# Performance work log

Measured on AMD Instinct MI355X. Metric: run time of the kernel, lower is better.

The kernel has to match this reference:

```python
import jax, jax.numpy as jnp
import numpy as np

DROPOUT_P = 0.5


def setup_inputs() -> dict:
    key = jax.random.key(0)
    ks = jax.random.split(key, 8)
    N, F0 = 10000, 1024
    s = lambda k, shp, fan: jax.random.normal(k, shp, jnp.float32) / np.sqrt(fan)
    return {
        "x": jax.random.normal(ks[0], (N, F0), jnp.float32),
        "adj": jax.random.uniform(ks[1], (N, N), jnp.float32),
        "W1": s(ks[2], (F0, 512), F0),
        "b1": jnp.zeros((512,), jnp.float32),
        "W2": s(ks[3], (512, 256), 512),
        "b2": jnp.zeros((256,), jnp.float32),
        "W3": s(ks[4], (256, 128), 256),
        "b3": jnp.zeros((128,), jnp.float32),
    }


def _gc(x, adj, W, b):
    # GraphConvolution: adj @ (x @ W) + b
    return adj @ (x @ W) + b


def reference(x, adj, W1, b1, W2, b2, W3, b3):
    x1 = jax.nn.relu(_gc(x, adj, W1, b1))
    # F.dropout(x1, p) with training=True: mask + 1/(1-p) scaling; fixed key for determinism
    keep = jax.random.bernoulli(jax.random.key(42), 1.0 - DROPOUT_P, x1.shape)
    x1 = jnp.where(keep, x1 / (1.0 - DROPOUT_P), 0.0)
    x2 = _gc(x1, adj, W2, b2)
    x3 = _gc(x2, adj, W3, b3)
    return x3
```

## Files before the change

kernel.cpp:

```cpp
#include <hip/hip_runtime.h>
#include <hip/hip_bf16.h>
#include <stdint.h>


#define MROWS 10000
#define KPAD  10016

typedef __attribute__((ext_vector_type(8))) short short8;
typedef __attribute__((ext_vector_type(4))) float floatx4;

__device__ __forceinline__ unsigned short f2bf(float f) {
  union { float f; unsigned u; } v; v.f = f;
  unsigned u = v.u;
  u += 0x7fffu + ((u >> 16) & 1u);
  return (unsigned short)(u >> 16);
}

__device__ __forceinline__ bool dropout_keep(unsigned i) {
  const unsigned halfn = 2560000u;
  const unsigned j = (i < halfn) ? i : (i - halfn);
  unsigned x0 = j, x1 = j + halfn;
  const unsigned k0 = 0u, k1 = 42u, k2 = 0u ^ 42u ^ 0x1BD11BDAu;
  x0 += k0; x1 += k1;
#define TFR(r) { x0 += x1; x1 = (x1 << (r)) | (x1 >> (32 - (r))); x1 ^= x0; }
  TFR(13) TFR(15) TFR(26) TFR(6)   x0 += k1; x1 += k2 + 1u;
  TFR(17) TFR(29) TFR(16) TFR(24)  x0 += k2; x1 += k0 + 2u;
  TFR(13) TFR(15) TFR(26) TFR(6)   x0 += k0; x1 += k1 + 3u;
  TFR(17) TFR(29) TFR(16) TFR(24)  x0 += k1; x1 += k2 + 4u;
  TFR(13) TFR(15) TFR(26) TFR(6)   x0 += k2; x1 += k0 + 5u;
#undef TFR
  const unsigned bits = (i < halfn) ? x0 : x1;
  return bits < 0x80000000u;
}

__global__ void cast_adj_kernel(const float* __restrict__ in, unsigned short* __restrict__ out) {
  const int q = blockIdx.x * blockDim.x + threadIdx.x;
  const int row = blockIdx.y;
  if (q >= 2504) return;
  const int col = q * 4;
  ushort4 o;
  if (col < 10000) {
    const float4 v = *(const float4*)(in + (size_t)row * 10000 + col);
    o.x = f2bf(v.x); o.y = f2bf(v.y); o.z = f2bf(v.z); o.w = f2bf(v.w);
  } else {
    o.x = 0; o.y = 0; o.z = 0; o.w = 0;
  }
  *(ushort4*)(out + (size_t)row * KPAD + col) = o;
}

__global__ void cast_vec_kernel(const float* __restrict__ in, unsigned short* __restrict__ out, int n4) {
  const int id = blockIdx.x * blockDim.x + threadIdx.x;
  if (id >= n4) return;
  const float4 v = ((const float4*)in)[id];
  ushort4 o; o.x = f2bf(v.x); o.y = f2bf(v.y); o.z = f2bf(v.z); o.w = f2bf(v.w);
  ((ushort4*)out)[id] = o;
}

__global__ void castT_kernel(const float* __restrict__ in, unsigned short* __restrict__ out, int K, int N) {
  const int id = blockIdx.x * blockDim.x + threadIdx.x;
  if (id >= K * N) return;
  const int n = id / K, k = id % K;
  out[(size_t)n * K + k] = f2bf(in[(size_t)k * N + n]);
}

__global__ void zero_pad_kernel(unsigned short* __restrict__ p, int rows) {
  const int id = blockIdx.x * blockDim.x + threadIdx.x;
  if (id >= rows * 16) return;
  const int r = id >> 4, c = id & 15;
  p[(size_t)r * KPAD + 10000 + c] = 0;
}

template<int OUT_KIND, int EPI>
__global__ __launch_bounds__(256, 2) void gemm_mfma(
    const unsigned short* __restrict__ A, int lda,
    const unsigned short* __restrict__ BT, int ldb,
    void* __restrict__ Cv, int ldc,
    const float* __restrict__ bias,
    int M, int N, int K,
    int chunk)
{
  __shared__ unsigned short As[128 * 32];
  __shared__ unsigned short Bs[128 * 32];

  const int tid  = threadIdx.x;
  const int lane = tid & 63;
  const int wave = tid >> 6;
  const int m0 = blockIdx.y * 128;
  const int n0 = blockIdx.x * 128;
  const int wm = (wave & 1) * 64;
  const int wn = (wave >> 1) * 64;

  int kstart = 0, kend = K;
  if (OUT_KIND == 3) {
    kstart = blockIdx.z * chunk;
    kend   = kstart + chunk; if (kend > K) kend = K;
  }

  floatx4 acc[4][4];
#pragma unroll
  for (int i = 0; i < 4; ++i)
#pragma unroll
    for (int j = 0; j < 4; ++j) acc[i][j] = (floatx4){0.f, 0.f, 0.f, 0.f};

  const int c1 = tid, c2 = tid + 256;
  int ar1 = m0 + (c1 >> 2); if (ar1 > M - 1) ar1 = M - 1;
  int ar2 = m0 + (c2 >> 2); if (ar2 > M - 1) ar2 = M - 1;
  const int br1 = n0 + (c1 >> 2);
  const int br2 = n0 + (c2 >> 2);
  const unsigned short* aG1 = A  + (size_t)ar1 * lda + (c1 & 3) * 8;
  const unsigned short* aG2 = A  + (size_t)ar2 * lda + (c2 & 3) * 8;
  const unsigned short* bG1 = BT + (size_t)br1 * ldb + (c1 & 3) * 8;
  const unsigned short* bG2 = BT + (size_t)br2 * ldb + (c2 & 3) * 8;
  unsigned short* lA1 = As + c1 * 8;
  unsigned short* lA2 = As + c2 * 8;
  unsigned short* lB1 = Bs + c1 * 8;
  unsigned short* lB2 = Bs + c2 * 8;

  const int fr = lane & 15;
  const int fq = (lane >> 4) * 8;

#define GLL16(g, l) __builtin_amdgcn_global_load_lds( \
    (const __attribute__((address_space(1))) void*)(g), \
    (__attribute__((address_space(3))) void*)(l), 16, 0, 0)

  for (int k0 = kstart; k0 < kend; k0 += 32) {
    GLL16(aG1 + k0, lA1);
    GLL16(aG2 + k0, lA2);
    GLL16(bG1 + k0, lB1);
    GLL16(bG2 + k0, lB2);
    __syncthreads();
    short8 af[4], bfv[4];
#pragma unroll
    for (int mi = 0; mi < 4; ++mi)
      af[mi] = *(const short8*)(As + (wm + mi * 16 + fr) * 32 + fq);
#pragma unroll
    for (int ni = 0; ni < 4; ++ni)
      bfv[ni] = *(const short8*)(Bs + (wn + ni * 16 + fr) * 32 + fq);
#pragma unroll
    for (int mi = 0; mi < 4; ++mi)
#pragma unroll
      for (int ni = 0; ni < 4; ++ni)
        acc[mi][ni] = __builtin_amdgcn_mfma_f32_16x16x32_bf16(af[mi], bfv[ni], acc[mi][ni], 0, 0, 0);
    __syncthreads();
  }
#undef GLL16

  if (OUT_KIND == 0) {
    unsigned short* Ct = (unsigned short*)Cv;
#pragma unroll
    for (int mi = 0; mi < 4; ++mi) {
      const int mbase = m0 + wm + mi * 16 + (lane >> 4) * 4;
      if (mbase < M) {
#pragma unroll
        for (int ni = 0; ni < 4; ++ni) {
          const int n = n0 + wn + ni * 16 + fr;
          ushort4 o;
          o.x = f2bf(acc[mi][ni][0]);
          o.y = f2bf(acc[mi][ni][1]);
          o.z = f2bf(acc[mi][ni][2]);
          o.w = f2bf(acc[mi][ni][3]);
          *(ushort4*)(Ct + (size_t)n * ldc + mbase) = o;
        }
      }
    }
  } else if (OUT_KIND == 3) {
    float* P = (float*)Cv + (size_t)blockIdx.z * (size_t)M * (size_t)N;
#pragma unroll
    for (int ni = 0; ni < 4; ++ni) {
      const int col = n0 + wn + ni * 16 + fr;
#pragma unroll
      for (int mi = 0; mi < 4; ++mi) {
        const int rbase = m0 + wm + mi * 16 + (lane >> 4) * 4;
#pragma unroll
        for (int r = 0; r < 4; ++r) {
          const int row = rbase + r;
          if (row < M) P[(size_t)row * N + col] = acc[mi][ni][r];
        }
      }
    }
  } else {
#pragma unroll
    for (int ni = 0; ni < 4; ++ni) {
      const int col = n0 + wn + ni * 16 + fr;
      const float bv = (EPI >= 1) ? bias[col] : 0.0f;
#pragma unroll
      for (int mi = 0; mi < 4; ++mi) {
        const int rbase = m0 + wm + mi * 16 + (lane >> 4) * 4;
#pragma unroll
        for (int r = 0; r < 4; ++r) {
          const int row = rbase + r;
          if (row < M) {
            float v = acc[mi][ni][r] + bv;
            if (EPI == 2) {
              v = v > 0.f ? v : 0.f;
              const unsigned idx = (unsigned)row * (unsigned)N + (unsigned)col;
              v = dropout_keep(idx) ? v * 2.0f : 0.0f;
            }
            if (OUT_KIND == 2)
              ((float*)Cv)[(size_t)row * ldc + col] = v;
            else
              ((unsigned short*)Cv)[(size_t)row * ldc + col] = f2bf(v);
          }
        }
      }
    }
  }
}

template<int EPI>
__global__ void reduce_epi_kernel(const float* __restrict__ P, void* __restrict__ outv,
                                  const float* __restrict__ bias,
                                  int S, int total4, unsigned nmask, size_t MN) {
  const int t = blockIdx.x * blockDim.x + threadIdx.x;
  if (t >= total4) return;
  const size_t off = (size_t)t * 4;
  float4 a = *(const float4*)(P + off);
  for (int s = 1; s < S; ++s) {
    const float4 b = *(const float4*)(P + (size_t)s * MN + off);
    a.x += b.x; a.y += b.y; a.z += b.z; a.w += b.w;
  }
  const unsigned col = (unsigned)off & nmask;
  a.x += bias[col]; a.y += bias[col + 1]; a.z += bias[col + 2]; a.w += bias[col + 3];
  if (EPI == 2) {
    float* e = &a.x;
#pragma unroll
    for (int j = 0; j < 4; ++j) {
      float v = e[j] > 0.f ? e[j] : 0.f;
      e[j] = dropout_keep((unsigned)off + j) ? v * 2.0f : 0.0f;
    }
  }
  if (EPI == 3) {
    *(float4*)((float*)outv + off) = a;
  } else {
    ushort4 o;
    o.x = f2bf(a.x); o.y = f2bf(a.y); o.z = f2bf(a.z); o.w = f2bf(a.w);
    *(ushort4*)((unsigned short*)outv + off) = o;
  }
}

static inline int pick_split(size_t avail, size_t per_split, int target) {
  int s = 1;
  while (s < target && (size_t)(s * 2) * per_split <= avail) s *= 2;
  return s;
}

extern "C" void kernel_launch(void* const* d_in, const int* in_sizes, int n_in,
                              void* d_out, int out_size, void* d_ws, size_t ws_size,
                              hipStream_t stream) {
  const float* x   = (const float*)d_in[0];
  const float* adj = (const float*)d_in[1];
  const float* W1  = (const float*)d_in[2];
  const float* b1  = (const float*)d_in[3];
  const float* W2  = (const float*)d_in[4];
  const float* b2  = (const float*)d_in[5];
  const float* W3  = (const float*)d_in[6];
  const float* b3  = (const float*)d_in[7];
  float* out = (float*)d_out;

  char* ws = (char*)d_ws;
  unsigned short* adjb = (unsigned short*)(ws);
  unsigned short* xb   = (unsigned short*)(ws + 200320000ull);
  unsigned short* w1t  = (unsigned short*)(ws + 220800000ull);
  unsigned short* w2t  = (unsigned short*)(ws + 221848576ull);
  unsigned short* w3t  = (unsigned short*)(ws + 222110720ull);
  unsigned short* h1t  = (unsigned short*)(ws + 222176256ull);
  unsigned short* x1   = (unsigned short*)(ws + 232432640ull);
  unsigned short* h2t  = (unsigned short*)(ws + 242672640ull);
  unsigned short* x2   = (unsigned short*)(ws + 247800832ull);
  unsigned short* h3t  = (unsigned short*)(ws + 252920832ull);
  float*          P    = (float*)(ws + 255484928ull);
  const size_t avail = (ws_size > 255484928ull) ? ws_size - 255484928ull : 0;

  const int S1 = pick_split(avail, 20480000ull, 4);
  const int S2 = pick_split(avail, 10240000ull, 8);
  const int S3 = pick_split(avail,  5120000ull, 16);

  cast_adj_kernel<<<dim3(10, 10000), 256, 0, stream>>>(adj, adjb);
  cast_vec_kernel<<<10000, 256, 0, stream>>>(x, xb, 2560000);
  castT_kernel<<<2048, 256, 0, stream>>>(W1, w1t, 1024, 512);
  castT_kernel<<<512, 256, 0, stream>>>(W2, w2t, 512, 256);
  castT_kernel<<<128, 256, 0, stream>>>(W3, w3t, 256, 128);
  zero_pad_kernel<<<32, 256, 0, stream>>>(h1t, 512);
  zero_pad_kernel<<<16, 256, 0, stream>>>(h2t, 256);
  zero_pad_kernel<<<8, 256, 0, stream>>>(h3t, 128);

  gemm_mfma<0, 0><<<dim3(4, 79), 256, 0, stream>>>(xb, 1024, w1t, 1024, h1t, KPAD, nullptr, MROWS, 512, 1024, 1024);

  if (S1 > 1) {
    const int chunk = ((313 + S1 - 1) / S1) * 32;
    gemm_mfma<3, 0><<<dim3(4, 79, S1), 256, 0, stream>>>(adjb, KPAD, h1t, KPAD, P, 512, nullptr, MROWS, 512, KPAD, chunk);
    reduce_epi_kernel<2><<<5000, 256, 0, stream>>>(P, x1, b1, S1, 1280000, 511u, 5120000ull);
  } else {
    gemm_mfma<1, 2><<<dim3(4, 79), 256, 0, stream>>>(adjb, KPAD, h1t, KPAD, x1, 512, b1, MROWS, 512, KPAD, KPAD);
  }

  gemm_mfma<0, 0><<<dim3(2, 79), 256, 0, stream>>>(x1, 512, w2t, 512, h2t, KPAD, nullptr, MROWS, 256, 512, 512);

  if (S2 > 1) {
    const int chunk = ((313 + S2 - 1) / S2) * 32;
    gemm_mfma<3, 0><<<dim3(2, 79, S2), 256, 0, stream>>>(adjb, KPAD, h2t, KPAD, P, 256, nullptr, MROWS, 256, KPAD, chunk);
    reduce_epi_kernel<1><<<2500, 256, 0, stream>>>(P, x2, b2, S2, 640000, 255u, 2560000ull);
  } else {
    gemm_mfma<1, 1><<<dim3(2, 79), 256, 0, stream>>>(adjb, KPAD, h2t, KPAD, x2, 256, b2, MROWS, 256, KPAD, KPAD);
  }

  gemm_mfma<0, 0><<<dim3(1, 79), 256, 0, stream>>>(x2, 256, w3t, 256, h3t, KPAD, nullptr, MROWS, 128, 256, 256);

  if (S3 > 1) {
    const int chunk = ((313 + S3 - 1) / S3) * 32;
    gemm_mfma<3, 0><<<dim3(1, 79, S3), 256, 0, stream>>>(adjb, KPAD, h3t, KPAD, P, 128, nullptr, MROWS, 128, KPAD, chunk);
    reduce_epi_kernel<3><<<1250, 256, 0, stream>>>(P, out, b3, S3, 320000, 127u, 1280000ull);
  } else {
    gemm_mfma<2, 1><<<dim3(1, 79), 256, 0, stream>>>(adjb, KPAD, h3t, KPAD, out, 128, b3, MROWS, 128, KPAD, KPAD);
  }
}
```

Measured before the change: 1.119 ms.

## Add 256x256 double-buffered split-K GEMM for the two large adjacency products

```diff
diff --git a/kernel.cpp b/kernel.cpp
--- a/kernel.cpp
+++ b/kernel.cpp
@@ -4,7 +4,7 @@
 
 
 #define MROWS 10000
-#define KPAD  10016
+#define KPAD  10048
 
 typedef __attribute__((ext_vector_type(8))) short short8;
 typedef __attribute__((ext_vector_type(4))) float floatx4;
@@ -36,7 +36,7 @@
 __global__ void cast_adj_kernel(const float* __restrict__ in, unsigned short* __restrict__ out) {
   const int q = blockIdx.x * blockDim.x + threadIdx.x;
   const int row = blockIdx.y;
-  if (q >= 2504) return;
+  if (q >= 2512) return;
   const int col = q * 4;
   ushort4 o;
   if (col < 10000) {
@@ -65,8 +65,8 @@
 
 __global__ void zero_pad_kernel(unsigned short* __restrict__ p, int rows) {
   const int id = blockIdx.x * blockDim.x + threadIdx.x;
-  if (id >= rows * 16) return;
-  const int r = id >> 4, c = id & 15;
+  if (id >= rows * 48) return;
+  const int r = id / 48, c = id % 48;
   p[(size_t)r * KPAD + 10000 + c] = 0;
 }
 
@@ -207,6 +207,163 @@
   }
 }
 
+__device__ __forceinline__ void bar_sync() {
+  asm volatile("" ::: "memory");
+  __builtin_amdgcn_s_barrier();
+  asm volatile("" ::: "memory");
+}
+#define WAITV(N) asm volatile("s_waitcnt vmcnt(" #N ")" ::: "memory")
+
+__global__ __launch_bounds__(512, 2) void gemm8p(
+    const unsigned short* __restrict__ A, int lda,
+    const unsigned short* __restrict__ BT, int ldb,
+    float* __restrict__ P,
+    int M, int N, int K, int chunk)
+{
+  __shared__ unsigned short As[2][256 * 64];
+  __shared__ unsigned short Bs[2][256 * 64];
+
+  const int tid  = threadIdx.x;
+  const int lane = tid & 63;
+  const int wave = tid >> 6;
+  const int wr = (wave >> 2) * 128;
+  const int wc = (wave & 3) * 64;
+  const int fr  = lane & 15;
+  const int fq4 = lane >> 4;
+
+  const int gx = gridDim.x, gy = gridDim.y;
+  int bid = blockIdx.x + gx * (blockIdx.y + gy * blockIdx.z);
+  const int nwg = gx * gy * gridDim.z;
+  if ((nwg & 7) == 0) bid = (bid & 7) * (nwg >> 3) + (bid >> 3);
+  const int bx = bid % gx;
+  const int t1 = bid / gx;
+  const int by = t1 % gy;
+  const int bz = t1 / gy;
+
+  const int m0 = by * 256;
+  const int n0 = bx * 256;
+  int kstart = bz * chunk;
+  int kend   = kstart + chunk; if (kend > K) kend = K;
+
+  floatx4 acc[8][4];
+#pragma unroll
+  for (int i = 0; i < 8; ++i)
+#pragma unroll
+    for (int j = 0; j < 4; ++j) acc[i][j] = (floatx4){0.f, 0.f, 0.f, 0.f};
+
+  const int srow = tid >> 3;
+  const int g8   = (tid & 7) * 8;
+  const int gsw  = ((tid & 7) ^ (srow & 7)) * 8;
+  const int d00 = (srow      ) * 64 + g8;
+  const int d01 = (srow +  64) * 64 + g8;
+  const int d10 = (srow + 128) * 64 + g8;
+  const int d11 = (srow + 192) * 64 + g8;
+  int ra00 = m0 + srow;        if (ra00 > M - 1) ra00 = M - 1;
+  int ra01 = m0 + srow +  64;  if (ra01 > M - 1) ra01 = M - 1;
+  int ra10 = m0 + srow + 128;  if (ra10 > M - 1) ra10 = M - 1;
+  int ra11 = m0 + srow + 192;  if (ra11 > M - 1) ra11 = M - 1;
+  const unsigned short* aS00 = A  + (size_t)ra00 * lda + gsw;
+  const unsigned short* aS01 = A  + (size_t)ra01 * lda + gsw;
+  const unsigned short* aS10 = A  + (size_t)ra10 * lda + gsw;
+  const unsigned short* aS11 = A  + (size_t)ra11 * lda + gsw;
+  const unsigned short* bS00 = BT + (size_t)(n0 + srow      ) * ldb + gsw;
+  const unsigned short* bS01 = BT + (size_t)(n0 + srow +  64) * ldb + gsw;
+  const unsigned short* bS10 = BT + (size_t)(n0 + srow + 128) * ldb + gsw;
+  const unsigned short* bS11 = BT + (size_t)(n0 + srow + 192) * ldb + gsw;
+
+#define GLL(g, l) __builtin_amdgcn_global_load_lds( \
+    (const __attribute__((address_space(1))) void*)(g), \
+    (__attribute__((address_space(3))) void*)(l), 16, 0, 0)
+
+#define RDA_HALF(mh) do { \
+  _Pragma("unroll") for (int mi2 = 0; mi2 < 4; ++mi2) \
+  _Pragma("unroll") for (int kh = 0; kh < 2; ++kh) \
+    af[mi2][kh] = *(const short8*)(curA + (wr + (mh)*64 + mi2*16 + fr) * 64 \
+                                        + (((kh*4 + fq4) ^ (fr & 7)) * 8)); \
+} while (0)
+#define RDB_HALF(nh) do { \
+  _Pragma("unroll") for (int ni2 = 0; ni2 < 2; ++ni2) \
+  _Pragma("unroll") for (int kh = 0; kh < 2; ++kh) \
+    bf[(nh)*2 + ni2][kh] = *(const short8*)(curB + (wc + (nh)*32 + ni2*16 + fr) * 64 \
+                                                 + (((kh*4 + fq4) ^ (fr & 7)) * 8)); \
+} while (0)
+#define MFMAQ(mh, nh) do { \
+  __builtin_amdgcn_s_setprio(1); \
+  _Pragma("unroll") for (int mi2 = 0; mi2 < 4; ++mi2) \
+  _Pragma("unroll") for (int ni2 = 0; ni2 < 2; ++ni2) \
+  _Pragma("unroll") for (int kh = 0; kh < 2; ++kh) \
+    acc[(mh)*4 + mi2][(nh)*2 + ni2] = __builtin_amdgcn_mfma_f32_16x16x32_bf16( \
+        af[mi2][kh], bf[(nh)*2 + ni2][kh], acc[(mh)*4 + mi2][(nh)*2 + ni2], 0, 0, 0); \
+  __builtin_amdgcn_s_setprio(0); \
+} while (0)
+
+  if (kstart < kend) {
+    GLL(aS00 + kstart, As[0] + d00);
+    GLL(aS01 + kstart, As[0] + d01);
+    GLL(bS00 + kstart, Bs[0] + d00);
+    GLL(bS01 + kstart, Bs[0] + d01);
+    GLL(bS10 + kstart, Bs[0] + d10);
+    GLL(bS11 + kstart, Bs[0] + d11);
+    GLL(aS10 + kstart, As[0] + d10);
+    GLL(aS11 + kstart, As[0] + d11);
+
+    int cur = 0;
+    for (int kt = kstart; kt < kend; kt += 64, cur ^= 1) {
+      const unsigned short* curA = As[cur];
+      const unsigned short* curB = Bs[cur];
+      unsigned short* nxA = As[cur ^ 1];
+      unsigned short* nxB = Bs[cur ^ 1];
+      const int kn = kt + 64;
+      const bool pre = (kn < kend);
+      short8 af[4][2];
+      short8 bf[4][2];
+
+      if (pre) { GLL(aS00 + kn, nxA + d00); GLL(aS01 + kn, nxA + d01); }
+      if (pre) { WAITV(6); } else { WAITV(4); }
+      bar_sync();
+      RDA_HALF(0);
+      RDB_HALF(0);
+      MFMAQ(0, 0);
+
+      if (pre) { GLL(bS00 + kn, nxB + d00); GLL(bS01 + kn, nxB + d01); }
+      if (pre) { WAITV(6); } else { WAITV(2); }
+      bar_sync();
+      RDB_HALF(1);
+      MFMAQ(0, 1);
+
+      if (pre) { GLL(bS10 + kn, nxB + d10); GLL(bS11 + kn, nxB + d11); }
+      if (pre) { WAITV(6); } else { WAITV(0); }
+      bar_sync();
+      RDA_HALF(1);
+      MFMAQ(1, 0);
+
+      if (pre) { GLL(aS10 + kn, nxA + d10); GLL(aS11 + kn, nxA + d11); }
+      bar_sync();
+      MFMAQ(1, 1);
+    }
+  }
+#undef GLL
+#undef RDA_HALF
+#undef RDB_HALF
+#undef MFMAQ
+
+  float* Pz = P + (size_t)bz * ((size_t)M * (size_t)N);
+#pragma unroll
+  for (int mi = 0; mi < 8; ++mi) {
+    const int rb = m0 + wr + mi * 16 + fq4 * 4;
+#pragma unroll
+    for (int r = 0; r < 4; ++r) {
+      const int row = rb + r;
+      if (row < M) {
+        float* pr = Pz + (size_t)row * N + n0 + wc + fr;
+#pragma unroll
+        for (int nj = 0; nj < 4; ++nj)
+          pr[nj * 16] = acc[mi][nj][r];
+      }
+    }
+  }
+}
+
 template<int EPI>
 __global__ void reduce_epi_kernel(const float* __restrict__ P, void* __restrict__ outv,
                                   const float* __restrict__ bias,
@@ -259,36 +416,33 @@
 
   char* ws = (char*)d_ws;
   unsigned short* adjb = (unsigned short*)(ws);
-  unsigned short* xb   = (unsigned short*)(ws + 200320000ull);
-  unsigned short* w1t  = (unsigned short*)(ws + 220800000ull);
-  unsigned short* w2t  = (unsigned short*)(ws + 221848576ull);
-  unsigned short* w3t  = (unsigned short*)(ws + 222110720ull);
-  unsigned short* h1t  = (unsigned short*)(ws + 222176256ull);
-  unsigned short* x1   = (unsigned short*)(ws + 232432640ull);
-  unsigned short* h2t  = (unsigned short*)(ws + 242672640ull);
-  unsigned short* x2   = (unsigned short*)(ws + 247800832ull);
-  unsigned short* h3t  = (unsigned short*)(ws + 252920832ull);
-  float*          P    = (float*)(ws + 255484928ull);
-  const size_t avail = (ws_size > 255484928ull) ? ws_size - 255484928ull : 0;
-
-  const int S1 = pick_split(avail, 20480000ull, 4);
-  const int S2 = pick_split(avail, 10240000ull, 8);
-  const int S3 = pick_split(avail,  5120000ull, 16);
+  unsigned short* xb   = (unsigned short*)(ws + 200960000ull);
+  unsigned short* w1t  = (unsigned short*)(ws + 221440000ull);
+  unsigned short* w2t  = (unsigned short*)(ws + 222488576ull);
+  unsigned short* w3t  = (unsigned short*)(ws + 222750720ull);
+  unsigned short* h1t  = (unsigned short*)(ws + 222816256ull);
+  unsigned short* x1   = (unsigned short*)(ws + 233105408ull);
+  unsigned short* h2t  = (unsigned short*)(ws + 243345408ull);
+  unsigned short* x2   = (unsigned short*)(ws + 248489984ull);
+  unsigned short* h3t  = (unsigned short*)(ws + 253609984ull);
+  float*          P    = (float*)(ws + 256182272ull);
+  const size_t avail = (ws_size > 256182272ull) ? ws_size - 256182272ull : 0;
 
   cast_adj_kernel<<<dim3(10, 10000), 256, 0, stream>>>(adj, adjb);
   cast_vec_kernel<<<10000, 256, 0, stream>>>(x, xb, 2560000);
   castT_kernel<<<2048, 256, 0, stream>>>(W1, w1t, 1024, 512);
   castT_kernel<<<512, 256, 0, stream>>>(W2, w2t, 512, 256);
   castT_kernel<<<128, 256, 0, stream>>>(W3, w3t, 256, 128);
-  zero_pad_kernel<<<32, 256, 0, stream>>>(h1t, 512);
-  zero_pad_kernel<<<16, 256, 0, stream>>>(h2t, 256);
-  zero_pad_kernel<<<8, 256, 0, stream>>>(h3t, 128);
+  zero_pad_kernel<<<96, 256, 0, stream>>>(h1t, 512);
+  zero_pad_kernel<<<48, 256, 0, stream>>>(h2t, 256);
+  zero_pad_kernel<<<24, 256, 0, stream>>>(h3t, 128);
 
   gemm_mfma<0, 0><<<dim3(4, 79), 256, 0, stream>>>(xb, 1024, w1t, 1024, h1t, KPAD, nullptr, MROWS, 512, 1024, 1024);
 
-  if (S1 > 1) {
-    const int chunk = ((313 + S1 - 1) / S1) * 32;
-    gemm_mfma<3, 0><<<dim3(4, 79, S1), 256, 0, stream>>>(adjb, KPAD, h1t, KPAD, P, 512, nullptr, MROWS, 512, KPAD, chunk);
+  if (avail >= 20480000ull) {
+    const int S1 = pick_split(avail, 20480000ull, 8);
+    const int chunk = ((157 + S1 - 1) / S1) * 64;
+    gemm8p<<<dim3(2, 40, S1), 512, 0, stream>>>(adjb, KPAD, h1t, KPAD, P, MROWS, 512, KPAD, chunk);
     reduce_epi_kernel<2><<<5000, 256, 0, stream>>>(P, x1, b1, S1, 1280000, 511u, 5120000ull);
   } else {
     gemm_mfma<1, 2><<<dim3(4, 79), 256, 0, stream>>>(adjb, KPAD, h1t, KPAD, x1, 512, b1, MROWS, 512, KPAD, KPAD);
@@ -296,9 +450,10 @@
 
   gemm_mfma<0, 0><<<dim3(2, 79), 256, 0, stream>>>(x1, 512, w2t, 512, h2t, KPAD, nullptr, MROWS, 256, 512, 512);
 
-  if (S2 > 1) {
-    const int chunk = ((313 + S2 - 1) / S2) * 32;
-    gemm_mfma<3, 0><<<dim3(2, 79, S2), 256, 0, stream>>>(adjb, KPAD, h2t, KPAD, P, 256, nullptr, MROWS, 256, KPAD, chunk);
+  if (avail >= 10240000ull) {
+    const int S2 = pick_split(avail, 10240000ull, 16);
+    const int chunk = ((157 + S2 - 1) / S2) * 64;
+    gemm8p<<<dim3(1, 40, S2), 512, 0, stream>>>(adjb, KPAD, h2t, KPAD, P, MROWS, 256, KPAD, chunk);
     reduce_epi_kernel<1><<<2500, 256, 0, stream>>>(P, x2, b2, S2, 640000, 255u, 2560000ull);
   } else {
     gemm_mfma<1, 1><<<dim3(2, 79), 256, 0, stream>>>(adjb, KPAD, h2t, KPAD, x2, 256, b2, MROWS, 256, KPAD, KPAD);
@@ -306,8 +461,9 @@
 
   gemm_mfma<0, 0><<<dim3(1, 79), 256, 0, stream>>>(x2, 256, w3t, 256, h3t, KPAD, nullptr, MROWS, 128, 256, 256);
 
-  if (S3 > 1) {
-    const int chunk = ((313 + S3 - 1) / S3) * 32;
+  if (avail >= 5120000ull) {
+    const int S3 = pick_split(avail, 5120000ull, 16);
+    const int chunk = ((314 + S3 - 1) / S3) * 32;
     gemm_mfma<3, 0><<<dim3(1, 79, S3), 256, 0, stream>>>(adjb, KPAD, h3t, KPAD, P, 128, nullptr, MROWS, 128, KPAD, chunk);
     reduce_epi_kernel<3><<<1250, 256, 0, stream>>>(P, out, b3, S3, 320000, 127u, 1280000ull);
   } else {
```

After: 1.044 ms. -6.8%, faster.
